# Kernel optimization log

Hardware: AMD Instinct MI355X
Metric: run time of the kernel (lower is better)

Reference implementation:

```python
import jax, jax.numpy as jnp
import numpy as np

G = 8      # num_codebooks
D = 64     # codebook_dim
V = 1024   # codebook_size
BETA = 1.0


def setup_inputs() -> dict:
    key = jax.random.key(0)
    k1, k2, k3 = jax.random.split(key, 3)
    inputs = jax.random.normal(k1, (8, 2048, G * D), dtype=jnp.float32)
    paddings = jax.random.randint(k2, (8, 2048), 0, 2, dtype=jnp.int32)
    codebook = jax.random.normal(k3, (V, G, D), dtype=jnp.float32)
    return {"inputs": inputs, "paddings": paddings, "codebook": codebook}


def reference(inputs, paddings, codebook):
    B, T, _ = inputs.shape
    x = inputs.reshape(B, T, G, D)

    # Per-group L2 nearest neighbor: dist[b,t,g,v] = ||x - c||^2
    # ||x||^2 is constant over v, drop it for the argmin.
    dots = jnp.einsum("btgd,vgd->btgv", x, codebook)          # [B,T,G,V]
    c_sq = jnp.sum(codebook * codebook, axis=-1)                # [V,G]
    dists = c_sq.T[None, None] - 2.0 * dots                     # [B,T,G,V]
    ids = jnp.argmin(dists, axis=-1)                            # [B,T,G]

    # Gather selected codes per group.
    quantized = codebook[ids, jnp.arange(G)[None, None, :]]     # [B,T,G,D]

    mask = (1.0 - paddings.astype(jnp.float32))[:, :, None, None]  # [B,T,1,1]
    denom = mask.sum()
    xd = jax.lax.stop_gradient(x)
    qd = jax.lax.stop_gradient(quantized)
    kmeans_loss = jnp.sum((quantized - xd) ** 2 * mask) / denom
    commitment_loss = jnp.sum((x - qd) ** 2 * mask) / denom
    total_loss = kmeans_loss + BETA * commitment_loss

    # Straight-through estimator, masked.
    quantized_st = (x + jax.lax.stop_gradient(quantized - x)) * mask
    quantized_st = quantized_st.reshape(B, T, G * D)

    ids = jnp.where(mask[:, :, :, 0] == 0.0, -1, ids)           # [B,T,G]
    return ids, quantized_st, kmeans_loss, commitment_loss, total_loss
```

## Files before the change

kernel.cpp:

```cpp
#include <hip/hip_runtime.h>
#include <cfloat>
#include <stdint.h>

#define G_ 8
#define D_ 64
#define V_ 1024
#define BT_ 16384
#define TPB_ 256
#define NSLOT_ 128
#define TOKS_ 128
#define NC_ 64
#define NB_ 4
#define NCHUNK_ (V_ / NC_)

typedef unsigned long long u64;
typedef uint32_t u32;
typedef _Float16 h8 __attribute__((ext_vector_type(8)));
typedef float f32x4 __attribute__((ext_vector_type(4)));

typedef __attribute__((address_space(3))) uint32_t lds_u32;
typedef __attribute__((address_space(1))) uint32_t glb_u32;

#define GL2LDS(gsrc, ldst) \
    __builtin_amdgcn_global_load_lds((glb_u32*)(gsrc), (lds_u32*)(ldst), 16, 0, 0)


__global__ __launch_bounds__(256) void prep_csq(
        const float* __restrict__ cb, const int* __restrict__ pad,
        float* __restrict__ csqT,
        int* __restrict__ cnt, int* __restrict__ list,
        float* __restrict__ out_ids, float* __restrict__ out_q,
        _Float16* __restrict__ cbH, _Float16* __restrict__ cbL) {
    const int tid = threadIdx.x;
    const int bx  = blockIdx.x;
    const int lane = tid & 63, w = tid >> 6;

    {
        const int gid = bx * 256 + tid;
        const int row = gid >> 3;
        const int seg = gid & 7;
        const int v   = row >> 3, gg = row & 7;
        const float4* r = (const float4*)(cb + (size_t)row * 64 + seg * 8);
        float4 c0 = r[0], c1 = r[1];
        float xs[8] = {c0.x, c0.y, c0.z, c0.w, c1.x, c1.y, c1.z, c1.w};
        h8 hv, lv;
        float s = 0.f;
#pragma unroll
        for (int e = 0; e < 8; ++e) {
            s += xs[e] * xs[e];
            _Float16 hh = (_Float16)xs[e];
            hv[e] = hh;
            lv[e] = (_Float16)((xs[e] - (float)hh) * 4096.f);
        }
        const size_t dst = ((size_t)gg * V_ + v) * 64 + seg * 8;
        *(h8*)(cbH + dst) = hv;
        *(h8*)(cbL + dst) = lv;
        s += __shfl_xor(s, 1, 64);
        s += __shfl_xor(s, 2, 64);
        s += __shfl_xor(s, 4, 64);
        if (seg == 0) csqT[gg * V_ + v] = s;
    }

    __shared__ int s_plist[64];
    __shared__ int s_npl;
    if (w == 0) {
        int tok = bx * 64 + lane;
        bool active = (pad[tok] == 0);
        u64 bal = __ballot(active);
        int na  = __popcll(bal);
        int base = 0;
        if (lane == 0) base = atomicAdd(cnt, na);
        base = __shfl(base, 0, 64);
        const u64 mb = ((u64)1 << lane) - 1;
        if (active) list[base + __popcll(bal & mb)] = tok;
        else        s_plist[__popcll(~bal & mb)] = tok;
        if (lane == 0) s_npl = 64 - na;
    }
    __syncthreads();

    const int npl = s_npl;
    for (int i = w; i < npl; i += 4) {
        int tok = s_plist[i];
        float4 z = make_float4(0.f, 0.f, 0.f, 0.f);
        float4* q = (float4*)(out_q + (size_t)tok * (G_ * D_)) + lane * 2;
        q[0] = z;
        q[1] = z;
        if (lane < G_) out_ids[(size_t)tok * G_ + lane] = -1.0f;
    }
}

__global__ __launch_bounds__(TPB_, 2) void vq_scan(
    const float* __restrict__ inp,
    const float* __restrict__ cb,
    const float* __restrict__ csqT,
    const int* __restrict__ cnt,
    const int* __restrict__ list,
    const _Float16* __restrict__ cbH,
    const _Float16* __restrict__ cbL,
    float* __restrict__ out_ids,
    float* __restrict__ out_q,
    float* __restrict__ part) {

    __shared__ __align__(16) unsigned char BH[NB_][NC_ * 128];
    __shared__ __align__(16) unsigned char BL[NB_][NC_ * 128];
    __shared__ float csq_s[V_];
    __shared__ u64 merge_s[2][TOKS_];

    const int nact = cnt[0];
    const int tile = blockIdx.x;
    if (tile * TOKS_ >= nact) return;
    const int g    = blockIdx.y;
    const int tid  = threadIdx.x;
    const int lane = tid & 63;
    const int w    = tid >> 6;
    const int mh   = w >> 1;
    const int nh   = w & 1;
    const int r16  = lane & 15;
    const int kq   = lane >> 4;

    h8 AH[4][2], AL[4][2];
#pragma unroll
    for (int rf = 0; rf < 4; ++rf) {
        int p = tile * TOKS_ + mh * 64 + rf * 16 + r16;
        int tok = list[p < nact ? p : 0];
        const float* xr = inp + (size_t)tok * (G_ * D_) + g * D_;
#pragma unroll
        for (int kf = 0; kf < 2; ++kf) {
            const float4* xp = (const float4*)(xr + kf * 32 + kq * 8);
            float4 a = xp[0], b = xp[1];
            float xs[8] = {a.x, a.y, a.z, a.w, b.x, b.y, b.z, b.w};
#pragma unroll
            for (int e = 0; e < 8; ++e) {
                _Float16 hh = (_Float16)xs[e];
                AH[rf][kf][e] = hh;
                AL[rf][kf][e] = (_Float16)((xs[e] - (float)hh) * 4096.f);
            }
        }
    }

    const size_t soff = (size_t)(w * 16 + (lane >> 3)) * 128
                      + (size_t)(((lane & 7) ^ (lane >> 3)) * 16);
    const unsigned char* sH = (const unsigned char*)cbH + (size_t)g * 131072 + soff;
    const unsigned char* sL = (const unsigned char*)cbL + (size_t)g * 131072 + soff;
    const int ldsb = w * 2048;

#pragma unroll
    for (int c0 = 0; c0 < 3; ++c0) {
        const size_t adv = (size_t)c0 * 8192;
        GL2LDS(sH + adv,        &BH[c0][ldsb]);
        GL2LDS(sH + adv + 1024, &BH[c0][ldsb + 1024]);
        GL2LDS(sL + adv,        &BL[c0][ldsb]);
        GL2LDS(sL + adv + 1024, &BL[c0][ldsb + 1024]);
    }

    csq_s[tid]       = csqT[g * V_ + tid];
    csq_s[tid + 256] = csqT[g * V_ + tid + 256];
    csq_s[tid + 512] = csqT[g * V_ + tid + 512];
    csq_s[tid + 768] = csqT[g * V_ + tid + 768];

    float beste[16];
    int   bestid[16];
#pragma unroll
    for (int s = 0; s < 16; ++s) { beste[s] = -FLT_MAX / 2; bestid[s] = 0; }

    asm volatile("s_waitcnt lgkmcnt(0)" ::: "memory");

    const u32 o0 = (u32)((((nh * 32 + r16) * 128 + kq * 16))
                         ^ ((u32)(r16 & 7) << 4));

#pragma unroll 1
    for (int c = 0; c < NCHUNK_; ++c) {
        if (c < NCHUNK_ - 2)
            asm volatile("s_waitcnt vmcnt(8)\n\ts_barrier" ::: "memory");
        else if (c == NCHUNK_ - 2)
            asm volatile("s_waitcnt vmcnt(4)\n\ts_barrier" ::: "memory");
        else
            asm volatile("s_waitcnt vmcnt(0)\n\ts_barrier" ::: "memory");
        __builtin_amdgcn_sched_barrier(0);

        if (c + 3 < NCHUNK_) {
            const int b = (c + 3) & (NB_ - 1);
            const size_t adv = (size_t)(c + 3) * 8192;
            GL2LDS(sH + adv,        &BH[b][ldsb]);
            GL2LDS(sH + adv + 1024, &BH[b][ldsb + 1024]);
            GL2LDS(sL + adv,        &BL[b][ldsb]);
            GL2LDS(sL + adv + 1024, &BL[b][ldsb + 1024]);
        }

        const unsigned char* BHc = &BH[c & (NB_ - 1)][0];
        const unsigned char* BLc = &BL[c & (NB_ - 1)][0];
#pragma unroll
        for (int cf = 0; cf < 2; ++cf) {
            const u32 ob = o0 + (u32)(cf * 2048);
            const h8 bh0 = *(const h8*)(BHc + ob);
            const h8 bh1 = *(const h8*)(BHc + (ob ^ 64));
            const h8 bl0 = *(const h8*)(BLc + ob);
            const h8 bl1 = *(const h8*)(BLc + (ob ^ 64));
            const int vcol = c * NC_ + nh * 32 + cf * 16 + r16;
            const float ai = -0.5f * csq_s[vcol];
#pragma unroll
            for (int rf = 0; rf < 4; ++rf) {
                f32x4 a  = {ai, ai, ai, ai};
                f32x4 ac = {0.f, 0.f, 0.f, 0.f};
                a  = __builtin_amdgcn_mfma_f32_16x16x32_f16(AH[rf][0], bh0, a,  0, 0, 0);
                a  = __builtin_amdgcn_mfma_f32_16x16x32_f16(AH[rf][1], bh1, a,  0, 0, 0);
                ac = __builtin_amdgcn_mfma_f32_16x16x32_f16(AH[rf][0], bl0, ac, 0, 0, 0);
                ac = __builtin_amdgcn_mfma_f32_16x16x32_f16(AH[rf][1], bl1, ac, 0, 0, 0);
                ac = __builtin_amdgcn_mfma_f32_16x16x32_f16(AL[rf][0], bh0, ac, 0, 0, 0);
                ac = __builtin_amdgcn_mfma_f32_16x16x32_f16(AL[rf][1], bh1, ac, 0, 0, 0);
#pragma unroll
                for (int q = 0; q < 4; ++q) {
                    float e = fmaf(0x1.0p-12f, ac[q], a[q]);
                    int s = rf * 4 + q;
                    if (e > beste[s]) { beste[s] = e; bestid[s] = vcol; }
                }
            }
        }
    }

#pragma unroll
    for (int s = 0; s < 16; ++s) {
        float d = -2.f * beste[s];
        u32 u = __float_as_uint(d);
        u = u ^ ((u >> 31) ? 0xFFFFFFFFu : 0x80000000u);
        u64 pk = ((u64)u << 32) | (u32)bestid[s];
#pragma unroll
        for (int off = 1; off <= 8; off <<= 1) {
            u64 o = __shfl_xor(pk, off, 64);
            pk = (o < pk) ? o : pk;
        }
        if (r16 == 0) {
            int row = mh * 64 + (s >> 2) * 16 + kq * 4 + (s & 3);
            merge_s[nh][row] = pk;
        }
    }
    __syncthreads();

    float l = 0.f;
    {
        int tl = tid >> 1, qv = tid & 1;
        int p  = tile * TOKS_ + tl;
        if (p < nact) {
            int tok = list[p];
            u64 qa = merge_s[0][tl], qb = merge_s[1][tl];
            u64 qm = (qb < qa) ? qb : qa;
            int id  = (int)(qm & 0xFFFFFFFFull);
            const float4* cr = (const float4*)(cb + ((size_t)id * G_ + g) * D_) + qv * 8;
            const float4* xr = (const float4*)(inp + (size_t)tok * (G_ * D_) + g * D_) + qv * 8;
            float4* qo = (float4*)(out_q + (size_t)tok * (G_ * D_) + g * D_) + qv * 8;
#pragma unroll
            for (int k = 0; k < 8; ++k) {
                float4 cc = cr[k], xx = xr[k];
                float dx = cc.x - xx.x, dy = cc.y - xx.y;
                float dz = cc.z - xx.z, dw = cc.w - xx.w;
                l += dx * dx + dy * dy + dz * dz + dw * dw;
                qo[k] = cc;
            }
            if (qv == 0) out_ids[(size_t)tok * G_ + g] = (float)id;
        }
    }
#pragma unroll
    for (int off = 32; off > 0; off >>= 1) l += __shfl_down(l, off, 64);
    if (lane == 0) {
        int slot = ((blockIdx.y * gridDim.x + blockIdx.x) * 4 + w) & (NSLOT_ - 1);
        atomicAdd(&part[slot], l);
    }
}

__global__ void finalize_kernel(const float* __restrict__ part,
                                const int* __restrict__ cnt,
                                float* __restrict__ out_losses) {
    int lane = threadIdx.x;
    float l = part[lane] + part[lane + 64];
#pragma unroll
    for (int off = 32; off > 0; off >>= 1) l += __shfl_down(l, off, 64);
    if (lane == 0) {
        float k = l / (float)cnt[0];
        out_losses[0] = k;
        out_losses[1] = k;
        out_losses[2] = 2.f * k;
    }
}

extern "C" void kernel_launch(void* const* d_in, const int* in_sizes, int n_in,
                              void* d_out, int out_size, void* d_ws, size_t ws_size,
                              hipStream_t stream) {
    const float* inp = (const float*)d_in[0];
    const int*   pad = (const int*)d_in[1];
    const float* cb  = (const float*)d_in[2];

    float* out   = (float*)d_out;
    float* o_ids = out;
    float* o_q   = out + (size_t)BT_ * G_;
    float* o_ls  = o_q + (size_t)BT_ * G_ * D_;

    float*     part = (float*)d_ws;
    int*       cnt  = (int*)((char*)d_ws + 512);
    float*     csqT = (float*)((char*)d_ws + 1024);
    int*       list = (int*)((char*)d_ws + 33792);
    _Float16*  cbH  = (_Float16*)((char*)d_ws + 131072);
    _Float16*  cbL  = (_Float16*)((char*)d_ws + 131072 + 1048576);

    hipMemsetAsync(d_ws, 0, 1024, stream);

    prep_csq<<<dim3(256), dim3(256), 0, stream>>>(
        cb, pad, csqT, cnt, list, o_ids, o_q, cbH, cbL);

    dim3 grid(BT_ / TOKS_, G_);
    vq_scan<<<grid, dim3(TPB_), 0, stream>>>(
        inp, cb, csqT, cnt, list, cbH, cbL, o_ids, o_q, part);

    finalize_kernel<<<1, dim3(64), 0, stream>>>(part, cnt, o_ls);
}
```

Baseline: 127.9 us.

## Give each wave a private codebook LDS slice and drop per-chunk block barriers

Each wave now loads only the half of each codebook chunk its column half (nh) needs into its own private LDS region. Buffering drops from four shared buffers to two per wave, and the per-chunk s_barrier is replaced with per-wave vmcnt waits, which removes block-wide synchronisation from the scan loop. The cost is duplicated global-to-LDS traffic, since waves sharing an nh load the same data, and a shallower prefetch of one chunk ahead instead of three.

```diff
diff --git a/kernel.cpp b/kernel.cpp
--- a/kernel.cpp
+++ b/kernel.cpp
@@ -10,7 +10,6 @@
 #define NSLOT_ 128
 #define TOKS_ 128
 #define NC_ 64
-#define NB_ 4
 #define NCHUNK_ (V_ / NC_)
 
 typedef unsigned long long u64;
@@ -101,8 +100,8 @@
     float* __restrict__ out_q,
     float* __restrict__ part) {
 
-    __shared__ __align__(16) unsigned char BH[NB_][NC_ * 128];
-    __shared__ __align__(16) unsigned char BL[NB_][NC_ * 128];
+    __shared__ __align__(16) unsigned char BH[2][4][4096];
+    __shared__ __align__(16) unsigned char BL[2][4][4096];
     __shared__ float csq_s[V_];
     __shared__ u64 merge_s[2][TOKS_];
 
@@ -138,20 +137,17 @@
         }
     }
 
-    const size_t soff = (size_t)(w * 16 + (lane >> 3)) * 128
+    const size_t soff = (size_t)(lane >> 3) * 128
                       + (size_t)(((lane & 7) ^ (lane >> 3)) * 16);
-    const unsigned char* sH = (const unsigned char*)cbH + (size_t)g * 131072 + soff;
-    const unsigned char* sL = (const unsigned char*)cbL + (size_t)g * 131072 + soff;
-    const int ldsb = w * 2048;
-
-#pragma unroll
-    for (int c0 = 0; c0 < 3; ++c0) {
-        const size_t adv = (size_t)c0 * 8192;
-        GL2LDS(sH + adv,        &BH[c0][ldsb]);
-        GL2LDS(sH + adv + 1024, &BH[c0][ldsb + 1024]);
-        GL2LDS(sL + adv,        &BL[c0][ldsb]);
-        GL2LDS(sL + adv + 1024, &BL[c0][ldsb + 1024]);
-    }
+    const unsigned char* sH = (const unsigned char*)cbH
+                            + (size_t)g * 131072 + (size_t)nh * 4096 + soff;
+    const unsigned char* sL = (const unsigned char*)cbL
+                            + (size_t)g * 131072 + (size_t)nh * 4096 + soff;
+
+#pragma unroll
+    for (int i = 0; i < 4; ++i) GL2LDS(sH + i * 1024, &BH[0][0][0] + (size_t)w * 4096 + i * 1024);
+#pragma unroll
+    for (int i = 0; i < 4; ++i) GL2LDS(sL + i * 1024, &BL[0][0][0] + (size_t)w * 4096 + i * 1024);
 
     csq_s[tid]       = csqT[g * V_ + tid];
     csq_s[tid + 256] = csqT[g * V_ + tid + 256];
@@ -163,32 +159,31 @@
 #pragma unroll
     for (int s = 0; s < 16; ++s) { beste[s] = -FLT_MAX / 2; bestid[s] = 0; }
 
-    asm volatile("s_waitcnt lgkmcnt(0)" ::: "memory");
-
-    const u32 o0 = (u32)((((nh * 32 + r16) * 128 + kq * 16))
-                         ^ ((u32)(r16 & 7) << 4));
+    __syncthreads();
+
+    const u32 o0 = (u32)(((r16 * 128 + kq * 16)) ^ ((u32)(r16 & 7) << 4));
 
 #pragma unroll 1
     for (int c = 0; c < NCHUNK_; ++c) {
-        if (c < NCHUNK_ - 2)
-            asm volatile("s_waitcnt vmcnt(8)\n\ts_barrier" ::: "memory");
-        else if (c == NCHUNK_ - 2)
-            asm volatile("s_waitcnt vmcnt(4)\n\ts_barrier" ::: "memory");
-        else
-            asm volatile("s_waitcnt vmcnt(0)\n\ts_barrier" ::: "memory");
+        asm volatile("s_waitcnt lgkmcnt(0)" ::: "memory");
+
+        if (c + 1 < NCHUNK_) {
+            const int b = (c + 1) & 1;
+            const size_t adv = (size_t)(c + 1) * 8192;
+            unsigned char* dH = &BH[b][0][0] + (size_t)w * 4096;
+            unsigned char* dL = &BL[b][0][0] + (size_t)w * 4096;
+#pragma unroll
+            for (int i = 0; i < 4; ++i) GL2LDS(sH + adv + i * 1024, dH + i * 1024);
+#pragma unroll
+            for (int i = 0; i < 4; ++i) GL2LDS(sL + adv + i * 1024, dL + i * 1024);
+            asm volatile("s_waitcnt vmcnt(8)" ::: "memory");
+        } else {
+            asm volatile("s_waitcnt vmcnt(0)" ::: "memory");
+        }
         __builtin_amdgcn_sched_barrier(0);
 
-        if (c + 3 < NCHUNK_) {
-            const int b = (c + 3) & (NB_ - 1);
-            const size_t adv = (size_t)(c + 3) * 8192;
-            GL2LDS(sH + adv,        &BH[b][ldsb]);
-            GL2LDS(sH + adv + 1024, &BH[b][ldsb + 1024]);
-            GL2LDS(sL + adv,        &BL[b][ldsb]);
-            GL2LDS(sL + adv + 1024, &BL[b][ldsb + 1024]);
-        }
-
-        const unsigned char* BHc = &BH[c & (NB_ - 1)][0];
-        const unsigned char* BLc = &BL[c & (NB_ - 1)][0];
+        const unsigned char* BHc = &BH[c & 1][0][0] + (size_t)w * 4096;
+        const unsigned char* BLc = &BL[c & 1][0][0] + (size_t)w * 4096;
 #pragma unroll
         for (int cf = 0; cf < 2; ++cf) {
             const u32 ob = o0 + (u32)(cf * 2048);
```

New measurement: 131.2 us. 2.6% more time.
